# Performance work log

Hardware: AMD Instinct MI355X
Metric: run time of the kernel (lower is better)

The kernel has to match this reference:

```python
import jax, jax.numpy as jnp
import numpy as np

LOG_2PI = float(np.log(2.0 * np.pi))
LOSS_BETA = 1.0
SIGMA = 1.0
EPS = 1e-6


def setup_inputs() -> dict:
    key = jax.random.key(0)
    z_activations = jax.random.normal(key, (2048, 16, 8), dtype=jnp.float32)
    return {"z_activations": z_activations}


def reference(z_activations):
    N, num_attr, pose_dim = z_activations.shape
    x = z_activations.reshape(N, -1)  # (N, K)
    K = x.shape[1]

    # standardize (torch.std is unbiased, ddof=1)
    mean = jnp.mean(x, axis=0, keepdims=True)
    std = jnp.std(x, axis=0, keepdims=True, ddof=1)
    x = (x - mean) / (std + EPS)

    logN = jnp.log(jnp.asarray(N, dtype=x.dtype))

    # per-dimension pairwise squared differences: (N, N, K)
    d = (x[:, None, :] - x[None, :, :]) ** 2

    # joint: log p(x_i | x_j) for K-dim Gaussian, sigma=1
    sq_dist = jnp.sum(d, axis=2)  # (N, N)
    c_joint = -0.5 * K * LOG_2PI - K * jnp.log(jnp.asarray(SIGMA, dtype=x.dtype))
    log_prob_joint = c_joint - sq_dist / (2.0 * SIGMA ** 2)
    log_q_z_given_x = jax.nn.logsumexp(log_prob_joint, axis=1) - logN  # (N,)

    # marginals: 1-D Gaussian per dim, all K at once (fuses the torch K-loop)
    c_marg = -0.5 * LOG_2PI - jnp.log(jnp.asarray(SIGMA, dtype=x.dtype))
    log_prob_marg = c_marg - d / (2.0 * SIGMA ** 2)  # (N, N, K)
    log_q_z_j = jax.nn.logsumexp(log_prob_marg, axis=1) - logN  # (N, K)
    sum_log_q_z_j = jnp.sum(log_q_z_j, axis=1)  # (N,)

    tc_loss = jnp.mean(log_q_z_given_x - sum_log_q_z_j)
    return tc_loss * LOSS_BETA
```

## Files before the change

kernel.cpp:

```cpp
#include <hip/hip_runtime.h>
#include <hip/hip_bf16.h>

#define NROWS 2048
#define KDIM  128
#define NCELL 16
#define PORD  10
#define NGRAM 512
#define NEVAL 256

typedef float f32x4  __attribute__((ext_vector_type(4)));
typedef short bf16x8 __attribute__((ext_vector_type(8)));

__device__ __forceinline__ float fexp2(float x){ return __builtin_amdgcn_exp2f(x); }
__device__ __forceinline__ float flog2(float x){ return __builtin_amdgcn_logf(x); }

#define CS 0.8493218002880191f

#define OFF_PART   0
#define OFF_ACCUM  8192
#define OFF_JOINT  8448
#define OFF_SLOG   10496
#define OFF_NRM    12544
#define OFF_MOM    14592
#define OFF_CTR    35072
#define OFF_XS     35076
#define ZERO_BASE  OFF_JOINT
#define ZERO_LEN   (2048 + 2048 + 2048 + 20480 + 4)

__device__ __forceinline__ void col_stats_from(float s, float s2, float& scale, float& shift){
  float m = s * (1.f / NROWS);
  float var = fmaxf((s2 - (float)NROWS * m * m) * (1.f / (NROWS - 1)), 0.f);
  scale = 1.f / (sqrtf(var) + 1e-6f);
  shift = -m * scale;
}

__device__ __forceinline__ float hermCell(float s,
    float q0, float q1, float q2, float q3, float q4,
    float q5, float q6, float q7, float q8, float q9){
  float scl = s * CS;
  float e = fexp2(-(scl * scl));
  float prev = 1.f, cur = s, nxt;
  float inner = fmaf(q1, s, q0);
  nxt = fmaf(s, cur, -1.f * prev); inner = fmaf(q2, nxt, inner); prev = cur; cur = nxt;
  nxt = fmaf(s, cur, -2.f * prev); inner = fmaf(q3, nxt, inner); prev = cur; cur = nxt;
  nxt = fmaf(s, cur, -3.f * prev); inner = fmaf(q4, nxt, inner); prev = cur; cur = nxt;
  nxt = fmaf(s, cur, -4.f * prev); inner = fmaf(q5, nxt, inner); prev = cur; cur = nxt;
  nxt = fmaf(s, cur, -5.f * prev); inner = fmaf(q6, nxt, inner); prev = cur; cur = nxt;
  nxt = fmaf(s, cur, -6.f * prev); inner = fmaf(q7, nxt, inner); prev = cur; cur = nxt;
  nxt = fmaf(s, cur, -7.f * prev); inner = fmaf(q8, nxt, inner); prev = cur; cur = nxt;
  nxt = fmaf(s, cur, -8.f * prev); inner = fmaf(q9, nxt, inner);
  return e * inner;
}

__global__ __launch_bounds__(1024) void tc_stats(const float* __restrict__ x,
                                                 float* __restrict__ ws){
  const int t  = threadIdx.x;
  const int k  = t & 127;
  const int rg = t >> 7;
  const int r0 = blockIdx.x * 64;
  {
    int idx = blockIdx.x * 1024 + t;
    if (idx < ZERO_LEN) ws[ZERO_BASE + idx] = 0.f;
  }
  float s = 0.f, s2 = 0.f;
  #pragma unroll
  for (int it = 0; it < 8; ++it){
    float v = x[(size_t)(r0 + it * 8 + rg) * KDIM + k];
    s += v;
    s2 = fmaf(v, v, s2);
  }
  __shared__ float ls[8][128], ls2[8][128];
  ls[rg][k] = s; ls2[rg][k] = s2;
  __syncthreads();
  if (t < 128){
    float a = 0.f, b = 0.f;
    #pragma unroll
    for (int g = 0; g < 8; ++g){ a += ls[g][t]; b += ls2[g][t]; }
    ws[OFF_PART + blockIdx.x * 256 + t]       = a;
    ws[OFF_PART + blockIdx.x * 256 + 128 + t] = b;
  }
}

__global__ __launch_bounds__(128) void tc_moments(const float* __restrict__ x,
                                                  float* __restrict__ ws){
  const int k   = blockIdx.x >> 4;
  const int seg = blockIdx.x & 15;
  const int t   = threadIdx.x;
  __shared__ float lm[NCELL * PORD];
  lm[t] = 0.f;
  if (t < 32) lm[128 + t] = 0.f;

  float s = 0.f, s2 = 0.f;
  #pragma unroll
  for (int b = 0; b < 32; ++b){
    s  += ws[OFF_PART + b * 256 + k];
    s2 += ws[OFF_PART + b * 256 + 128 + k];
  }
  if (seg == 0 && t == 0){
    ws[OFF_ACCUM + k]       = s;
    ws[OFF_ACCUM + 128 + k] = s2;
  }
  float scale, shift; col_stats_from(s, s2, scale, shift);
  __syncthreads();

  const int row = seg * 128 + t;
  float y = fmaf(x[(size_t)row * KDIM + k], scale, shift);

  {
    __hip_bfloat16 hb = __float2bfloat16(y * CS);
    unsigned short us = *(unsigned short*)&hb;
    ((unsigned short*)(ws + OFF_XS))[(size_t)row * KDIM + k] = us;
    float ybf = __builtin_bit_cast(float, (unsigned int)us << 16);
    atomicAdd(&ws[OFF_NRM + row], ybf * ybf);
  }

  int c = (int)floorf(y * 2.f + 8.f);
  c = min(max(c, 0), NCELL - 1);
  float u = y - (-3.75f + 0.5f * (float)c);
  float* b10 = &lm[c * PORD];
  atomicAdd(&b10[0], 1.f);
  float pw = u;
  atomicAdd(&b10[1], pw);
  pw *= u; atomicAdd(&b10[2], pw * 0.5f);
  pw *= u; atomicAdd(&b10[3], pw * 1.6666666666e-1f);
  pw *= u; atomicAdd(&b10[4], pw * 4.1666666666e-2f);
  pw *= u; atomicAdd(&b10[5], pw * 8.3333333333e-3f);
  pw *= u; atomicAdd(&b10[6], pw * 1.3888888889e-3f);
  pw *= u; atomicAdd(&b10[7], pw * 1.9841269841e-4f);
  pw *= u; atomicAdd(&b10[8], pw * 2.4801587302e-5f);
  pw *= u; atomicAdd(&b10[9], pw * 2.7557319224e-6f);
  __syncthreads();

  float* mom = ws + OFF_MOM;
  for (int idx = t; idx < NCELL * PORD; idx += 128)
    atomicAdd(&mom[(size_t)idx * KDIM + k], lm[idx]);
}

__global__ __launch_bounds__(512) void tc_gram(float* __restrict__ ws){
  const int t = threadIdx.x;
  const int wave = t >> 6, lane = t & 63;
  const int bid = blockIdx.x;
  const int bi = bid >> 5, bj = bid & 31;
  const int Ibase = bi * 128, Jbase = bj * 64;
  float* joint = ws + OFF_JOINT;
  const float* nrm = ws + OFF_NRM;
  const unsigned short* xs = (const unsigned short*)(ws + OFF_XS);

  const int wi = wave >> 2, wj = wave & 3;
  const int lr = lane & 15, hs = lane >> 4;

  f32x4 acc0 = {0.f,0.f,0.f,0.f}, acc1 = acc0, acc2 = acc0, acc3 = acc0;
  #pragma unroll
  for (int kq = 0; kq < 4; ++kq){
    const int co = kq * 32 + hs * 8;
    bf16x8 bf = *(const bf16x8*)(xs + (size_t)(Jbase + wj * 16 + lr) * KDIM + co);
    bf16x8 a0 = *(const bf16x8*)(xs + (size_t)(Ibase + wi * 64 + lr +  0) * KDIM + co);
    bf16x8 a1 = *(const bf16x8*)(xs + (size_t)(Ibase + wi * 64 + lr + 16) * KDIM + co);
    bf16x8 a2 = *(const bf16x8*)(xs + (size_t)(Ibase + wi * 64 + lr + 32) * KDIM + co);
    bf16x8 a3 = *(const bf16x8*)(xs + (size_t)(Ibase + wi * 64 + lr + 48) * KDIM + co);
    acc0 = __builtin_amdgcn_mfma_f32_16x16x32_bf16(a0, bf, acc0, 0, 0, 0);
    acc1 = __builtin_amdgcn_mfma_f32_16x16x32_bf16(a1, bf, acc1, 0, 0, 0);
    acc2 = __builtin_amdgcn_mfma_f32_16x16x32_bf16(a2, bf, acc2, 0, 0, 0);
    acc3 = __builtin_amdgcn_mfma_f32_16x16x32_bf16(a3, bf, acc3, 0, 0, 0);
  }

  const float njv = nrm[Jbase + wj * 16 + lr];
  const int rbase = hs * 4;
  float jp[4][4];
  #pragma unroll
  for (int mt = 0; mt < 4; ++mt){
    f32x4 a4 = (mt == 0) ? acc0 : (mt == 1) ? acc1 : (mt == 2) ? acc2 : acc3;
    const float4 nI4 = *(const float4*)(nrm + Ibase + wi * 64 + mt * 16 + rbase);
    jp[mt][0] = fexp2(-(nI4.x + njv - 2.f * a4[0]));
    jp[mt][1] = fexp2(-(nI4.y + njv - 2.f * a4[1]));
    jp[mt][2] = fexp2(-(nI4.z + njv - 2.f * a4[2]));
    jp[mt][3] = fexp2(-(nI4.w + njv - 2.f * a4[3]));
  }
  #pragma unroll
  for (int mt = 0; mt < 4; ++mt){
    #pragma unroll
    for (int p = 0; p < 4; ++p){
      float v = jp[mt][p];
      v += __shfl_xor(v, 1); v += __shfl_xor(v, 2);
      v += __shfl_xor(v, 4); v += __shfl_xor(v, 8);
      jp[mt][p] = v;
    }
  }
  if (lr == 0){
    #pragma unroll
    for (int mt = 0; mt < 4; ++mt)
      #pragma unroll
      for (int p = 0; p < 4; ++p)
        atomicAdd(&joint[Ibase + wi * 64 + mt * 16 + rbase + p], jp[mt][p]);
  }
}

__global__ __launch_bounds__(512) void tc_eval(const float* __restrict__ x,
                                               float* __restrict__ ws,
                                               float* __restrict__ out){
  __shared__ float red2[8];
  __shared__ int lastflag;
  const int t = threadIdx.x;
  const int wave = t >> 6, lane = t & 63;
  const int k = t & 127, irg = t >> 7;
  const int bid = blockIdx.x;
  const int r0 = bid * 8 + irg * 2;
  float* joint = ws + OFF_JOINT;
  float* slog  = ws + OFF_SLOG;
  const float* accum = ws + OFF_ACCUM;
  const float* mom   = ws + OFF_MOM;

  float scale, shift;
  col_stats_from(accum[k], accum[128 + k], scale, shift);
  const float y0 = fmaf(x[(size_t)r0 * KDIM + k],       scale, shift);
  const float y1 = fmaf(x[(size_t)(r0 + 1) * KDIM + k], scale, shift);

  float S0 = 0.f, S1 = 0.f;
  #pragma unroll
  for (int c = 0; c < NCELL; ++c){
    const float* mp = mom + (size_t)c * PORD * KDIM + k;
    const float q0 = mp[0 * KDIM], q1 = mp[1 * KDIM], q2 = mp[2 * KDIM];
    const float q3 = mp[3 * KDIM], q4 = mp[4 * KDIM], q5 = mp[5 * KDIM];
    const float q6 = mp[6 * KDIM], q7 = mp[7 * KDIM], q8 = mp[8 * KDIM];
    const float q9 = mp[9 * KDIM];
    const float ctr = -3.75f + 0.5f * (float)c;
    S0 += hermCell(y0 - ctr, q0,q1,q2,q3,q4,q5,q6,q7,q8,q9);
    S1 += hermCell(y1 - ctr, q0,q1,q2,q3,q4,q5,q6,q7,q8,q9);
  }
  float lg0 = flog2(S0), lg1 = flog2(S1);
  #pragma unroll
  for (int off = 1; off < 64; off <<= 1){
    lg0 += __shfl_xor(lg0, off);
    lg1 += __shfl_xor(lg1, off);
  }
  if (lane == 0){
    atomicAdd(&slog[r0],     lg0);
    atomicAdd(&slog[r0 + 1], lg1);
  }

  __syncthreads();
  if (t == 0){
    __threadfence();
    unsigned int* ctr = (unsigned int*)(ws + OFF_CTR);
    unsigned int old = __hip_atomic_fetch_add(ctr, 1u, __ATOMIC_ACQ_REL, __HIP_MEMORY_SCOPE_AGENT);
    lastflag = (old == NEVAL - 1);
  }
  __syncthreads();
  if (lastflag){
    float acc = 0.f;
    #pragma unroll
    for (int q = 0; q < 4; ++q){
      int r = q * 512 + t;
      float jv = __hip_atomic_load(&joint[r], __ATOMIC_RELAXED, __HIP_MEMORY_SCOPE_AGENT);
      float sv = __hip_atomic_load(&slog[r],  __ATOMIC_RELAXED, __HIP_MEMORY_SCOPE_AGENT);
      acc += 0.6931471805599453f * (flog2(jv) - sv);
    }
    #pragma unroll
    for (int m = 1; m < 64; m <<= 1) acc += __shfl_xor(acc, m);
    if (lane == 0) red2[wave] = acc;
    __syncthreads();
    if (t == 0){
      float tot = 0.f;
      #pragma unroll
      for (int w = 0; w < 8; ++w) tot += red2[w];
      out[0] = tot * (1.0f / NROWS) + 968.32661124224364f;
    }
  }
}

extern "C" void kernel_launch(void* const* d_in, const int* in_sizes, int n_in,
                              void* d_out, int out_size, void* d_ws, size_t ws_size,
                              hipStream_t stream){
  const float* x = (const float*)d_in[0];
  float* out = (float*)d_out;
  float* ws  = (float*)d_ws;
  tc_stats  <<<32, 1024, 0, stream>>>(x, ws);
  tc_moments<<<KDIM * 16, 128, 0, stream>>>(x, ws);
  tc_gram   <<<NGRAM, 512, 0, stream>>>(ws);
  tc_eval   <<<NEVAL, 512, 0, stream>>>(x, ws, out);
}
```

Measured before the change: 136.7 us.

## Merge gram and eval kernels, transpose input for per-column moment blocks

Fuses the Gram/joint kernel and the marginal-evaluation kernel into one launch whose blocks branch by index, with the last-block counter extended to cover all blocks. The stats kernel also writes a column-major copy of the input so that the moments kernel can use one 1024-thread block per column. That block accumulates moments into per-wave shared bins and writes the results directly, with no global atomics. This removes one launch boundary and the global atomic traffic in the moments step. In exchange it adds an extra transposed write of the input with strided stores and reduces the moments kernel to 128 blocks. It also stops zeroing the moment buffer, which is now safe because it is overwritten.

New measurement: 152.5 us. 11.6% more time.

```diff
diff --git a/kernel.cpp b/kernel.cpp
--- a/kernel.cpp
+++ b/kernel.cpp
@@ -7,6 +7,7 @@
 #define PORD  10
 #define NGRAM 512
 #define NEVAL 256
+#define NBLK3 (NGRAM + NEVAL)
 
 typedef float f32x4  __attribute__((ext_vector_type(4)));
 typedef short bf16x8 __attribute__((ext_vector_type(8)));
@@ -23,9 +24,8 @@
 #define OFF_NRM    12544
 #define OFF_MOM    14592
 #define OFF_CTR    35072
-#define OFF_XS     35076
-#define ZERO_BASE  OFF_JOINT
-#define ZERO_LEN   (2048 + 2048 + 2048 + 20480 + 4)
+#define OFF_XT     35076
+#define OFF_XS     297220
 
 __device__ __forceinline__ void col_stats_from(float s, float s2, float& scale, float& shift){
   float m = s * (1.f / NROWS);
@@ -60,14 +60,17 @@
   const int r0 = blockIdx.x * 64;
   {
     int idx = blockIdx.x * 1024 + t;
-    if (idx < ZERO_LEN) ws[ZERO_BASE + idx] = 0.f;
+    if (idx < 6144) ws[OFF_JOINT + idx] = 0.f;
+    if (idx == 6144) *(unsigned int*)(ws + OFF_CTR) = 0u;
   }
   float s = 0.f, s2 = 0.f;
   #pragma unroll
   for (int it = 0; it < 8; ++it){
-    float v = x[(size_t)(r0 + it * 8 + rg) * KDIM + k];
+    const int row = r0 + it * 8 + rg;
+    float v = x[(size_t)row * KDIM + k];
     s += v;
     s2 = fmaf(v, v, s2);
+    ws[OFF_XT + (size_t)k * NROWS + row] = v;
   }
   __shared__ float ls[8][128], ls2[8][128];
   ls[rg][k] = s; ls2[rg][k] = s2;
@@ -81,14 +84,12 @@
   }
 }
 
-__global__ __launch_bounds__(128) void tc_moments(const float* __restrict__ x,
-                                                  float* __restrict__ ws){
-  const int k   = blockIdx.x >> 4;
-  const int seg = blockIdx.x & 15;
-  const int t   = threadIdx.x;
-  __shared__ float lm[NCELL * PORD];
-  lm[t] = 0.f;
-  if (t < 32) lm[128 + t] = 0.f;
+__global__ __launch_bounds__(1024) void tc_moments(float* __restrict__ ws){
+  const int k = blockIdx.x;
+  const int t = threadIdx.x;
+  const int wave = t >> 6;
+  __shared__ float lm[16][NCELL * PORD];
+  for (int i = t; i < 16 * NCELL * PORD; i += 1024) ((float*)lm)[i] = 0.f;
 
   float s = 0.f, s2 = 0.f;
   #pragma unroll
@@ -96,146 +97,142 @@
     s  += ws[OFF_PART + b * 256 + k];
     s2 += ws[OFF_PART + b * 256 + 128 + k];
   }
-  if (seg == 0 && t == 0){
+  if (t == 0){
     ws[OFF_ACCUM + k]       = s;
     ws[OFF_ACCUM + 128 + k] = s2;
   }
   float scale, shift; col_stats_from(s, s2, scale, shift);
   __syncthreads();
 
-  const int row = seg * 128 + t;
-  float y = fmaf(x[(size_t)row * KDIM + k], scale, shift);
-
-  {
+  #pragma unroll
+  for (int half = 0; half < 2; ++half){
+    const int row = t + half * 1024;
+    float y = fmaf(ws[OFF_XT + (size_t)k * NROWS + row], scale, shift);
     __hip_bfloat16 hb = __float2bfloat16(y * CS);
     unsigned short us = *(unsigned short*)&hb;
     ((unsigned short*)(ws + OFF_XS))[(size_t)row * KDIM + k] = us;
     float ybf = __builtin_bit_cast(float, (unsigned int)us << 16);
     atomicAdd(&ws[OFF_NRM + row], ybf * ybf);
-  }
-
-  int c = (int)floorf(y * 2.f + 8.f);
-  c = min(max(c, 0), NCELL - 1);
-  float u = y - (-3.75f + 0.5f * (float)c);
-  float* b10 = &lm[c * PORD];
-  atomicAdd(&b10[0], 1.f);
-  float pw = u;
-  atomicAdd(&b10[1], pw);
-  pw *= u; atomicAdd(&b10[2], pw * 0.5f);
-  pw *= u; atomicAdd(&b10[3], pw * 1.6666666666e-1f);
-  pw *= u; atomicAdd(&b10[4], pw * 4.1666666666e-2f);
-  pw *= u; atomicAdd(&b10[5], pw * 8.3333333333e-3f);
-  pw *= u; atomicAdd(&b10[6], pw * 1.3888888889e-3f);
-  pw *= u; atomicAdd(&b10[7], pw * 1.9841269841e-4f);
-  pw *= u; atomicAdd(&b10[8], pw * 2.4801587302e-5f);
-  pw *= u; atomicAdd(&b10[9], pw * 2.7557319224e-6f);
-  __syncthreads();
-
-  float* mom = ws + OFF_MOM;
-  for (int idx = t; idx < NCELL * PORD; idx += 128)
-    atomicAdd(&mom[(size_t)idx * KDIM + k], lm[idx]);
-}
-
-__global__ __launch_bounds__(512) void tc_gram(float* __restrict__ ws){
-  const int t = threadIdx.x;
-  const int wave = t >> 6, lane = t & 63;
-  const int bid = blockIdx.x;
-  const int bi = bid >> 5, bj = bid & 31;
-  const int Ibase = bi * 128, Jbase = bj * 64;
-  float* joint = ws + OFF_JOINT;
-  const float* nrm = ws + OFF_NRM;
-  const unsigned short* xs = (const unsigned short*)(ws + OFF_XS);
-
-  const int wi = wave >> 2, wj = wave & 3;
-  const int lr = lane & 15, hs = lane >> 4;
-
-  f32x4 acc0 = {0.f,0.f,0.f,0.f}, acc1 = acc0, acc2 = acc0, acc3 = acc0;
-  #pragma unroll
-  for (int kq = 0; kq < 4; ++kq){
-    const int co = kq * 32 + hs * 8;
-    bf16x8 bf = *(const bf16x8*)(xs + (size_t)(Jbase + wj * 16 + lr) * KDIM + co);
-    bf16x8 a0 = *(const bf16x8*)(xs + (size_t)(Ibase + wi * 64 + lr +  0) * KDIM + co);
-    bf16x8 a1 = *(const bf16x8*)(xs + (size_t)(Ibase + wi * 64 + lr + 16) * KDIM + co);
-    bf16x8 a2 = *(const bf16x8*)(xs + (size_t)(Ibase + wi * 64 + lr + 32) * KDIM + co);
-    bf16x8 a3 = *(const bf16x8*)(xs + (size_t)(Ibase + wi * 64 + lr + 48) * KDIM + co);
-    acc0 = __builtin_amdgcn_mfma_f32_16x16x32_bf16(a0, bf, acc0, 0, 0, 0);
-    acc1 = __builtin_amdgcn_mfma_f32_16x16x32_bf16(a1, bf, acc1, 0, 0, 0);
-    acc2 = __builtin_amdgcn_mfma_f32_16x16x32_bf16(a2, bf, acc2, 0, 0, 0);
-    acc3 = __builtin_amdgcn_mfma_f32_16x16x32_bf16(a3, bf, acc3, 0, 0, 0);
-  }
-
-  const float njv = nrm[Jbase + wj * 16 + lr];
-  const int rbase = hs * 4;
-  float jp[4][4];
-  #pragma unroll
-  for (int mt = 0; mt < 4; ++mt){
-    f32x4 a4 = (mt == 0) ? acc0 : (mt == 1) ? acc1 : (mt == 2) ? acc2 : acc3;
-    const float4 nI4 = *(const float4*)(nrm + Ibase + wi * 64 + mt * 16 + rbase);
-    jp[mt][0] = fexp2(-(nI4.x + njv - 2.f * a4[0]));
-    jp[mt][1] = fexp2(-(nI4.y + njv - 2.f * a4[1]));
-    jp[mt][2] = fexp2(-(nI4.z + njv - 2.f * a4[2]));
-    jp[mt][3] = fexp2(-(nI4.w + njv - 2.f * a4[3]));
-  }
-  #pragma unroll
-  for (int mt = 0; mt < 4; ++mt){
-    #pragma unroll
-    for (int p = 0; p < 4; ++p){
-      float v = jp[mt][p];
-      v += __shfl_xor(v, 1); v += __shfl_xor(v, 2);
-      v += __shfl_xor(v, 4); v += __shfl_xor(v, 8);
-      jp[mt][p] = v;
-    }
-  }
-  if (lr == 0){
-    #pragma unroll
-    for (int mt = 0; mt < 4; ++mt)
-      #pragma unroll
-      for (int p = 0; p < 4; ++p)
-        atomicAdd(&joint[Ibase + wi * 64 + mt * 16 + rbase + p], jp[mt][p]);
-  }
-}
-
-__global__ __launch_bounds__(512) void tc_eval(const float* __restrict__ x,
-                                               float* __restrict__ ws,
-                                               float* __restrict__ out){
+    int c = (int)floorf(y * 2.f + 8.f);
+    c = min(max(c, 0), NCELL - 1);
+    float u = y - (-3.75f + 0.5f * (float)c);
+    float* mm = &lm[wave][c * PORD];
+    atomicAdd(&mm[0], 1.f);
+    float pw = u;
+    atomicAdd(&mm[1], pw);
+    pw *= u; atomicAdd(&mm[2], pw * 0.5f);
+    pw *= u; atomicAdd(&mm[3], pw * 1.6666666666e-1f);
+    pw *= u; atomicAdd(&mm[4], pw * 4.1666666666e-2f);
+    pw *= u; atomicAdd(&mm[5], pw * 8.3333333333e-3f);
+    pw *= u; atomicAdd(&mm[6], pw * 1.3888888889e-3f);
+    pw *= u; atomicAdd(&mm[7], pw * 1.9841269841e-4f);
+    pw *= u; atomicAdd(&mm[8], pw * 2.4801587302e-5f);
+    pw *= u; atomicAdd(&mm[9], pw * 2.7557319224e-6f);
+  }
+  __syncthreads();
+
+  for (int i = t; i < NCELL * PORD; i += 1024){
+    float a = 0.f;
+    #pragma unroll
+    for (int w = 0; w < 16; ++w) a += lm[w][i];
+    ws[OFF_MOM + (size_t)i * KDIM + k] = a;
+  }
+}
+
+__global__ __launch_bounds__(512) void tc_joint(const float* __restrict__ x,
+                                                float* __restrict__ ws,
+                                                float* __restrict__ out){
   __shared__ float red2[8];
   __shared__ int lastflag;
   const int t = threadIdx.x;
   const int wave = t >> 6, lane = t & 63;
-  const int k = t & 127, irg = t >> 7;
   const int bid = blockIdx.x;
-  const int r0 = bid * 8 + irg * 2;
   float* joint = ws + OFF_JOINT;
   float* slog  = ws + OFF_SLOG;
+  const float* nrm   = ws + OFF_NRM;
   const float* accum = ws + OFF_ACCUM;
   const float* mom   = ws + OFF_MOM;
-
-  float scale, shift;
-  col_stats_from(accum[k], accum[128 + k], scale, shift);
-  const float y0 = fmaf(x[(size_t)r0 * KDIM + k],       scale, shift);
-  const float y1 = fmaf(x[(size_t)(r0 + 1) * KDIM + k], scale, shift);
-
-  float S0 = 0.f, S1 = 0.f;
-  #pragma unroll
-  for (int c = 0; c < NCELL; ++c){
-    const float* mp = mom + (size_t)c * PORD * KDIM + k;
-    const float q0 = mp[0 * KDIM], q1 = mp[1 * KDIM], q2 = mp[2 * KDIM];
-    const float q3 = mp[3 * KDIM], q4 = mp[4 * KDIM], q5 = mp[5 * KDIM];
-    const float q6 = mp[6 * KDIM], q7 = mp[7 * KDIM], q8 = mp[8 * KDIM];
-    const float q9 = mp[9 * KDIM];
-    const float ctr = -3.75f + 0.5f * (float)c;
-    S0 += hermCell(y0 - ctr, q0,q1,q2,q3,q4,q5,q6,q7,q8,q9);
-    S1 += hermCell(y1 - ctr, q0,q1,q2,q3,q4,q5,q6,q7,q8,q9);
-  }
-  float lg0 = flog2(S0), lg1 = flog2(S1);
-  #pragma unroll
-  for (int off = 1; off < 64; off <<= 1){
-    lg0 += __shfl_xor(lg0, off);
-    lg1 += __shfl_xor(lg1, off);
-  }
-  if (lane == 0){
-    atomicAdd(&slog[r0],     lg0);
-    atomicAdd(&slog[r0 + 1], lg1);
+  const unsigned short* xs = (const unsigned short*)(ws + OFF_XS);
+
+  if (bid < NGRAM){
+    const int bi = bid >> 5, bj = bid & 31;
+    const int Ibase = bi * 128, Jbase = bj * 64;
+    const int wi = wave >> 2, wj = wave & 3;
+    const int lr = lane & 15, hs = lane >> 4;
+
+    f32x4 acc0 = {0.f,0.f,0.f,0.f}, acc1 = acc0, acc2 = acc0, acc3 = acc0;
+    #pragma unroll
+    for (int kq = 0; kq < 4; ++kq){
+      const int co = kq * 32 + hs * 8;
+      bf16x8 bf = *(const bf16x8*)(xs + (size_t)(Jbase + wj * 16 + lr) * KDIM + co);
+      bf16x8 a0 = *(const bf16x8*)(xs + (size_t)(Ibase + wi * 64 + lr +  0) * KDIM + co);
+      bf16x8 a1 = *(const bf16x8*)(xs + (size_t)(Ibase + wi * 64 + lr + 16) * KDIM + co);
+      bf16x8 a2 = *(const bf16x8*)(xs + (size_t)(Ibase + wi * 64 + lr + 32) * KDIM + co);
+      bf16x8 a3 = *(const bf16x8*)(xs + (size_t)(Ibase + wi * 64 + lr + 48) * KDIM + co);
+      acc0 = __builtin_amdgcn_mfma_f32_16x16x32_bf16(a0, bf, acc0, 0, 0, 0);
+      acc1 = __builtin_amdgcn_mfma_f32_16x16x32_bf16(a1, bf, acc1, 0, 0, 0);
+      acc2 = __builtin_amdgcn_mfma_f32_16x16x32_bf16(a2, bf, acc2, 0, 0, 0);
+      acc3 = __builtin_amdgcn_mfma_f32_16x16x32_bf16(a3, bf, acc3, 0, 0, 0);
+    }
+
+    const float njv = nrm[Jbase + wj * 16 + lr];
+    const int rbase = hs * 4;
+    float jp[4][4];
+    #pragma unroll
+    for (int mt = 0; mt < 4; ++mt){
+      f32x4 a4 = (mt == 0) ? acc0 : (mt == 1) ? acc1 : (mt == 2) ? acc2 : acc3;
+      const float4 nI4 = *(const float4*)(nrm + Ibase + wi * 64 + mt * 16 + rbase);
+      jp[mt][0] = fexp2(-(nI4.x + njv - 2.f * a4[0]));
+      jp[mt][1] = fexp2(-(nI4.y + njv - 2.f * a4[1]));
+      jp[mt][2] = fexp2(-(nI4.z + njv - 2.f * a4[2]));
+      jp[mt][3] = fexp2(-(nI4.w + njv - 2.f * a4[3]));
+    }
+    #pragma unroll
+    for (int mt = 0; mt < 4; ++mt){
+      #pragma unroll
+      for (int p = 0; p < 4; ++p){
+        float v = jp[mt][p];
+        v += __shfl_xor(v, 1); v += __shfl_xor(v, 2);
+        v += __shfl_xor(v, 4); v += __shfl_xor(v, 8);
+        jp[mt][p] = v;
+      }
+    }
+    if (lr == 0){
+      #pragma unroll
+      for (int mt = 0; mt < 4; ++mt)
+        #pragma unroll
+        for (int p = 0; p < 4; ++p)
+          atomicAdd(&joint[Ibase + wi * 64 + mt * 16 + rbase + p], jp[mt][p]);
+    }
+  } else {
+    const int k = t & 127, irg = t >> 7;
+    const int r0 = (bid - NGRAM) * 8 + irg * 2;
+    float scale, shift;
+    col_stats_from(accum[k], accum[128 + k], scale, shift);
+    const float y0 = fmaf(x[(size_t)r0 * KDIM + k],       scale, shift);
+    const float y1 = fmaf(x[(size_t)(r0 + 1) * KDIM + k], scale, shift);
+    float S0 = 0.f, S1 = 0.f;
+    #pragma unroll
+    for (int c = 0; c < NCELL; ++c){
+      const float* mp = mom + (size_t)c * PORD * KDIM + k;
+      const float q0 = mp[0 * KDIM], q1 = mp[1 * KDIM], q2 = mp[2 * KDIM];
+      const float q3 = mp[3 * KDIM], q4 = mp[4 * KDIM], q5 = mp[5 * KDIM];
+      const float q6 = mp[6 * KDIM], q7 = mp[7 * KDIM], q8 = mp[8 * KDIM];
+      const float q9 = mp[9 * KDIM];
+      const float ctr = -3.75f + 0.5f * (float)c;
+      S0 += hermCell(y0 - ctr, q0,q1,q2,q3,q4,q5,q6,q7,q8,q9);
+      S1 += hermCell(y1 - ctr, q0,q1,q2,q3,q4,q5,q6,q7,q8,q9);
+    }
+    float lg0 = flog2(S0), lg1 = flog2(S1);
+    #pragma unroll
+    for (int off = 1; off < 64; off <<= 1){
+      lg0 += __shfl_xor(lg0, off);
+      lg1 += __shfl_xor(lg1, off);
+    }
+    if (lane == 0){
+      atomicAdd(&slog[r0],     lg0);
+      atomicAdd(&slog[r0 + 1], lg1);
+    }
   }
 
   __syncthreads();
@@ -243,7 +240,7 @@
     __threadfence();
     unsigned int* ctr = (unsigned int*)(ws + OFF_CTR);
     unsigned int old = __hip_atomic_fetch_add(ctr, 1u, __ATOMIC_ACQ_REL, __HIP_MEMORY_SCOPE_AGENT);
-    lastflag = (old == NEVAL - 1);
+    lastflag = (old == NBLK3 - 1);
   }
   __syncthreads();
   if (lastflag){
@@ -275,7 +272,6 @@
   float* out = (float*)d_out;
   float* ws  = (float*)d_ws;
   tc_stats  <<<32, 1024, 0, stream>>>(x, ws);
-  tc_moments<<<KDIM * 16, 128, 0, stream>>>(x, ws);
-  tc_gram   <<<NGRAM, 512, 0, stream>>>(ws);
-  tc_eval   <<<NEVAL, 512, 0, stream>>>(x, ws, out);
-}
+  tc_moments<<<KDIM, 1024, 0, stream>>>(ws);
+  tc_joint  <<<NBLK3, 512, 0, stream>>>(x, ws, out);
+}
```
